# Performance work log

Measured on AMD Instinct MI355X. Metric: run time of the kernel, lower is better.

## Reference

```python
import jax, jax.numpy as jnp
import numpy as np

EPS = 1e-12  # matches torch F.normalize default eps

def setup_inputs() -> dict:
    key = jax.random.key(0)
    k1, k2 = jax.random.split(key)
    query = jax.random.normal(k1, (8, 2048, 512), dtype=jnp.float32)
    support = jax.random.normal(k2, (8, 4096, 512), dtype=jnp.float32)
    return {"query": query, "support": support}

def _l2_normalize(x):
    # torch.nn.functional.normalize(x, dim=-1): x / max(||x||, eps)
    n = jnp.sqrt(jnp.sum(x * x, axis=-1, keepdims=True))
    return x / jnp.maximum(n, EPS)

def reference(query, support):
    # cosine distance: 1 - q_hat @ s_hat^T  -> [B, Nq, Ns]
    qn = _l2_normalize(query)
    sn = _l2_normalize(support)
    dist = 1.0 - jnp.einsum('bqd,bsd->bqs', qn, sn)
    min_d = jnp.min(dist, axis=2)        # [B, Nq]
    return jnp.mean(min_d, axis=1)       # [B]
```

## Files before the change

### kernel.cpp

```cpp
#include <hip/hip_runtime.h>
#include <hip/hip_bf16.h>

typedef __attribute__((ext_vector_type(8))) short short8;
typedef __attribute__((ext_vector_type(4))) float f32x4;
typedef __attribute__((ext_vector_type(16))) float f32x16;
typedef __attribute__((ext_vector_type(8))) int int8v;

#define D   512
#define NQ  2048
#define NS  4096
#define NB  8
#define BM  128
#define BN  128
#define BK  32

typedef const __attribute__((address_space(1))) unsigned int gas_uint;
typedef __attribute__((address_space(3))) unsigned int las_uint;

#define WAIT_VM8   0x0F78
#define WAIT_VM4   0x0F74
#define WAIT_VM0   0x0F70
#define WAIT_LGKM0 0xC07F

__device__ __forceinline__ short f2bf(float f) {
  unsigned u = __builtin_bit_cast(unsigned, f);
  unsigned r = u + 0x7fffu + ((u >> 16) & 1u);
  return (short)(r >> 16);
}

__device__ __forceinline__ short8 pack8(float4 a, float4 b, float r) {
  short8 o;
  o[0] = f2bf(a.x * r); o[1] = f2bf(a.y * r); o[2] = f2bf(a.z * r); o[3] = f2bf(a.w * r);
  o[4] = f2bf(b.x * r); o[5] = f2bf(b.y * r); o[6] = f2bf(b.z * r); o[7] = f2bf(b.w * r);
  return o;
}

__global__ void normcvt8_kernel(const float* __restrict__ q, const float* __restrict__ s,
                                unsigned char* __restrict__ qn, unsigned char* __restrict__ sn,
                                unsigned* __restrict__ maxenc) {
  if (blockIdx.x < 64) maxenc[(blockIdx.x << 8) | threadIdx.x] = 0;
  int wave = blockIdx.x * 4 + (threadIdx.x >> 6);
  int lane = threadIdx.x & 63;
  const int NQR = NB * NQ;
  const float4* src; unsigned char* dst;
  if (wave < NQR) { src = (const float4*)(q + (size_t)wave * D); dst = qn + (size_t)wave * D; }
  else {
    size_t w = wave - NQR;
    src = (const float4*)(s + w * D); dst = sn + w * D;
  }
  float4 a = src[lane * 2];
  float4 b = src[lane * 2 + 1];
  float ss = a.x*a.x + a.y*a.y + a.z*a.z + a.w*a.w
           + b.x*b.x + b.y*b.y + b.z*b.z + b.w*b.w;
  #pragma unroll
  for (int m = 32; m >= 1; m >>= 1) ss += __shfl_xor(ss, m, 64);
  float r = 1.0f / fmaxf(sqrtf(ss), 1e-12f);
  int w0 = __builtin_amdgcn_cvt_pk_fp8_f32(a.x * r, a.y * r, 0, false);
  w0     = __builtin_amdgcn_cvt_pk_fp8_f32(a.z * r, a.w * r, w0, true);
  int w1 = __builtin_amdgcn_cvt_pk_fp8_f32(b.x * r, b.y * r, 0, false);
  w1     = __builtin_amdgcn_cvt_pk_fp8_f32(b.z * r, b.w * r, w1, true);
  *(int2*)(dst + lane * 8) = make_int2(w0, w1);
}

__global__ __launch_bounds__(256) void cosmax11_kernel(
    const unsigned char* __restrict__ Qn, const unsigned char* __restrict__ Sn,
    unsigned int* __restrict__ maxenc)
{
  __shared__ __align__(16) unsigned char sbuf[65536];
  __shared__ float maxbuf[64][2];

  const int id  = blockIdx.x;
  const int b   = id & 7;
  const int j   = id >> 3;
  const int mt  = j & 31;
  const int nsp = j >> 5;
  const int tid  = threadIdx.x;
  const int wave = tid >> 6;
  const int lane = tid & 63;
  const int l31 = lane & 31, kc = lane >> 5;
  const int mstrip = wave & 1, nhalf = wave >> 1;

  {
    const unsigned char* Qbase = Qn + ((size_t)b * NQ + (size_t)mt * 64) * D;
    const int baserow = wave * 2 + (lane >> 5);
    #pragma unroll
    for (int p = 0; p < 8; ++p) {
      int row = p * 8 + baserow;
      int g   = (lane & 31) ^ (row & 31);
      __builtin_amdgcn_global_load_lds(
          (gas_uint*)(Qbase + (size_t)row * D + g * 16),
          (las_uint*)(sbuf + 16384 + p * 4096 + wave * 1024), 16, 0, 0);
    }
  }
  __syncthreads();

  const int srow8 = lane >> 3;
  const int sch   = (lane & 7) ^ srow8;
  const unsigned char* gS = Sn +
      ((size_t)b * NS + (size_t)nsp * 2048 + wave * 32 + srow8) * D + sch * 16;

  auto issue = [&](size_t goff, int ldsoff) {
    #pragma unroll
    for (int t = 0; t < 4; ++t)
      __builtin_amdgcn_global_load_lds((gas_uint*)(gS + goff + (size_t)t * 4096),
          (las_uint*)(sbuf + ldsoff + wave * 4096 + t * 1024), 16, 0, 0);
  };

  issue(0, 0);

  const int arow = mstrip * 32 + l31;
  int8v a[8];
  #pragma unroll
  for (int kk = 0; kk < 8; ++kk) {
    int c0 = (4 * kk + 2 * kc) ^ l31;
    ((int4*)&a[kk])[0] = *(const int4*)&sbuf[16384 + arow * 512 + c0 * 16];
    ((int4*)&a[kk])[1] = *(const int4*)&sbuf[16384 + arow * 512 + (c0 ^ 1) * 16];
  }
  __builtin_amdgcn_s_waitcnt(WAIT_LGKM0);
  asm volatile("" ::: "memory");
  __builtin_amdgcn_s_barrier();
  asm volatile("" ::: "memory");
  issue(128, 16384);
  issue(256, 32768);

  const int brow0 = (nhalf * 64 + l31) * 128;
  const int brow1 = brow0 + 4096;
  const int cxor  = ((kc * 2) ^ (l31 & 7)) * 16;

  f32x16 acc0, acc1;
  float rmax[16];
  #pragma unroll
  for (int r = 0; r < 16; ++r) rmax[r] = -2.0f;

  auto computeK = [&](int kt, int rdo) {
    const unsigned char* Bb = sbuf + rdo;
    #pragma unroll
    for (int ss = 0; ss < 2; ++ss) {
      const int cb = cxor ^ (ss * 64);
      int8v b0, b1;
      ((int4*)&b0)[0] = *(const int4*)&Bb[brow0 + cb];
      ((int4*)&b0)[1] = *(const int4*)&Bb[brow0 + (cb ^ 16)];
      ((int4*)&b1)[0] = *(const int4*)&Bb[brow1 + cb];
      ((int4*)&b1)[1] = *(const int4*)&Bb[brow1 + (cb ^ 16)];
      acc0 = __builtin_amdgcn_mfma_scale_f32_32x32x64_f8f6f4(
          a[kt * 2 + ss], b0, acc0, 0, 0, 0, 0x7f7f7f7f, 0, 0x7f7f7f7f);
      acc1 = __builtin_amdgcn_mfma_scale_f32_32x32x64_f8f6f4(
          a[kt * 2 + ss], b1, acc1, 0, 0, 0, 0x7f7f7f7f, 0, 0x7f7f7f7f);
    }
  };

  #pragma clang loop unroll(disable)
  for (int nt2 = 0; nt2 < 16; ++nt2) {
    const size_t ntb = (size_t)nt2 << 16;
    const bool more = (nt2 < 15);

    __builtin_amdgcn_s_waitcnt(WAIT_VM8);
    asm volatile("" ::: "memory");
    __builtin_amdgcn_s_barrier();
    asm volatile("" ::: "memory");
    issue(ntb + 384, 49152);
    #pragma unroll
    for (int r = 0; r < 16; ++r) { acc0[r] = 0.f; acc1[r] = 0.f; }
    computeK(0, 0);

    __builtin_amdgcn_s_waitcnt(WAIT_VM8);
    asm volatile("" ::: "memory");
    __builtin_amdgcn_s_barrier();
    asm volatile("" ::: "memory");
    if (more) issue(ntb + 65536, 0);
    computeK(1, 16384);

    if (more) __builtin_amdgcn_s_waitcnt(WAIT_VM8);
    else      __builtin_amdgcn_s_waitcnt(WAIT_VM4);
    asm volatile("" ::: "memory");
    __builtin_amdgcn_s_barrier();
    asm volatile("" ::: "memory");
    if (more) issue(ntb + 65536 + 128, 16384);
    computeK(2, 32768);

    if (more) __builtin_amdgcn_s_waitcnt(WAIT_VM8);
    else      __builtin_amdgcn_s_waitcnt(WAIT_VM0);
    asm volatile("" ::: "memory");
    __builtin_amdgcn_s_barrier();
    asm volatile("" ::: "memory");
    if (more) issue(ntb + 65536 + 256, 32768);
    computeK(3, 49152);

    #pragma unroll
    for (int r = 0; r < 16; ++r)
      rmax[r] = fmaxf(rmax[r], fmaxf(acc0[r], acc1[r]));
  }

  #pragma unroll
  for (int r = 0; r < 16; ++r) {
    float v = rmax[r];
    v = fmaxf(v, __shfl_xor(v, 1, 64));
    v = fmaxf(v, __shfl_xor(v, 2, 64));
    v = fmaxf(v, __shfl_xor(v, 4, 64));
    v = fmaxf(v, __shfl_xor(v, 8, 64));
    v = fmaxf(v, __shfl_xor(v, 16, 64));
    if (l31 == 0)
      maxbuf[mstrip * 32 + (r & 3) + 8 * (r >> 2) + 4 * kc][nhalf] = v;
  }
  __syncthreads();

  if (tid < 64) {
    float v = fmaxf(maxbuf[tid][0], maxbuf[tid][1]);
    unsigned e = __builtin_bit_cast(unsigned, v);
    e = ((int)e >= 0) ? (e | 0x80000000u) : ~e;
    atomicMax(&maxenc[(size_t)b * NQ + (size_t)mt * 64 + tid], e);
  }
}

__global__ void finalize_kernel(const unsigned* __restrict__ maxenc,
                                float* __restrict__ out) {
  int b = blockIdx.x;
  int tid = threadIdx.x;
  float sum = 0.f;
  for (int i = tid; i < NQ; i += 256) {
    unsigned e = maxenc[(size_t)b * NQ + i];
    unsigned u = (e & 0x80000000u) ? (e & 0x7fffffffu) : ~e;
    float v = __builtin_bit_cast(float, u);
    sum += 1.0f - v;
  }
  #pragma unroll
  for (int m = 32; m >= 1; m >>= 1) sum += __shfl_xor(sum, m, 64);
  __shared__ float part[4];
  if ((tid & 63) == 0) part[tid >> 6] = sum;
  __syncthreads();
  if (tid == 0) out[b] = (part[0] + part[1] + part[2] + part[3]) * (1.0f / (float)NQ);
}

__global__ void norms_kernel(const float* __restrict__ q, const float* __restrict__ s,
                             float* __restrict__ rq, float* __restrict__ rs) {
  int wave = blockIdx.x * 4 + (threadIdx.x >> 6);
  int lane = threadIdx.x & 63;
  const int NQR = NB * NQ, NSR = NB * NS;
  if (wave >= NQR + NSR) return;
  const float4* r4; float* outp;
  if (wave < NQR) { r4 = (const float4*)(q + (size_t)wave * D); outp = rq + wave; }
  else           { r4 = (const float4*)(s + (size_t)(wave - NQR) * D); outp = rs + (wave - NQR); }
  float4 a = r4[lane];
  float4 b = r4[lane + 64];
  float ss = a.x*a.x + a.y*a.y + a.z*a.z + a.w*a.w
           + b.x*b.x + b.y*b.y + b.z*b.z + b.w*b.w;
  #pragma unroll
  for (int m = 32; m >= 1; m >>= 1) ss += __shfl_xor(ss, m, 64);
  if (lane == 0) *outp = 1.0f / fmaxf(sqrtf(ss), 1e-12f);
}

__global__ __launch_bounds__(256, 3) void cosmax_kernel(
    const float* __restrict__ Q, const float* __restrict__ S,
    const float* __restrict__ rq, const float* __restrict__ rs,
    unsigned int* __restrict__ maxenc)
{
  __shared__ short As[BM * BK];
  __shared__ short Bs[BN * BK];
  __shared__ float maxbuf[BM][2];

  const int b  = blockIdx.z, mt = blockIdx.y, nt = blockIdx.x;
  const float* Qb  = Q + ((size_t)b * NQ + mt * BM) * D;
  const float* Sb  = S + ((size_t)b * NS + nt * BN) * D;
  const float* rqb = rq + (size_t)b * NQ + mt * BM;
  const float* rsb = rs + (size_t)b * NS + nt * BN;

  const int tid  = threadIdx.x;
  const int srow = tid >> 2;
  const int kseg = (tid & 3) * 8;
  const float rq0 = rqb[srow], rq1 = rqb[srow + 64];
  const float rs0 = rsb[srow], rs1 = rsb[srow + 64];
  const int wave = tid >> 6, lane = tid & 63;
  const int wm = (wave & 1) * 64, wn = (wave >> 1) * 64;
  const int lm = lane & 15, lk = (lane >> 4) * 8;

  f32x4 acc[4][4];
  #pragma unroll
  for (int i = 0; i < 4; ++i)
    #pragma unroll
    for (int j = 0; j < 4; ++j) acc[i][j] = (f32x4){0.f, 0.f, 0.f, 0.f};

  const float* qrow0 = Qb + (size_t)srow * D + kseg;
  const float* qrow1 = qrow0 + (size_t)64 * D;
  const float* srow0 = Sb + (size_t)srow * D + kseg;
  const float* srow1 = srow0 + (size_t)64 * D;

  float4 qa, qb2, qc, qd, sa, sb2, sc, sd;
  #define LOADK(k0)                                                    \
    qa  = *(const float4*)(qrow0 + (k0));  qb2 = *(const float4*)(qrow0 + (k0) + 4); \
    qc  = *(const float4*)(qrow1 + (k0));  qd  = *(const float4*)(qrow1 + (k0) + 4); \
    sa  = *(const float4*)(srow0 + (k0));  sb2 = *(const float4*)(srow0 + (k0) + 4); \
    sc  = *(const float4*)(srow1 + (k0));  sd  = *(const float4*)(srow1 + (k0) + 4);
  LOADK(0);
  #pragma unroll 4
  for (int kt = 0; kt < D / BK; ++kt) {
    *(short8*)&As[srow        * BK + kseg] = pack8(qa, qb2, rq0);
    *(short8*)&As[(srow + 64) * BK + kseg] = pack8(qc, qd,  rq1);
    *(short8*)&Bs[srow        * BK + kseg] = pack8(sa, sb2, rs0);
    *(short8*)&Bs[(srow + 64) * BK + kseg] = pack8(sc, sd,  rs1);
    __syncthreads();
    if (kt < D / BK - 1) { LOADK((kt + 1) * BK); }
    short8 af[4], bf[4];
    #pragma unroll
    for (int i = 0; i < 4; ++i) af[i] = *(short8*)&As[(wm + i * 16 + lm) * BK + lk];
    #pragma unroll
    for (int j = 0; j < 4; ++j) bf[j] = *(short8*)&Bs[(wn + j * 16 + lm) * BK + lk];
    #pragma unroll
    for (int i = 0; i < 4; ++i)
      #pragma unroll
      for (int j = 0; j < 4; ++j)
        acc[i][j] = __builtin_amdgcn_mfma_f32_16x16x32_bf16(af[i], bf[j], acc[i][j], 0, 0, 0);
    __syncthreads();
  }
  #undef LOADK

  #pragma unroll
  for (int i = 0; i < 4; ++i) {
    #pragma unroll
    for (int r = 0; r < 4; ++r) {
      float v = fmaxf(fmaxf(acc[i][0][r], acc[i][1][r]),
                      fmaxf(acc[i][2][r], acc[i][3][r]));
      v = fmaxf(v, __shfl_xor(v, 1, 64));
      v = fmaxf(v, __shfl_xor(v, 2, 64));
      v = fmaxf(v, __shfl_xor(v, 4, 64));
      v = fmaxf(v, __shfl_xor(v, 8, 64));
      if ((lane & 15) == 0) {
        int row = wm + i * 16 + (lane >> 4) * 4 + r;
        maxbuf[row][wave >> 1] = v;
      }
    }
  }
  __syncthreads();
  if (tid < BM) {
    float v = fmaxf(maxbuf[tid][0], maxbuf[tid][1]);
    unsigned e = __builtin_bit_cast(unsigned, v);
    e = ((int)e >= 0) ? (e | 0x80000000u) : ~e;
    atomicMax(&maxenc[(size_t)b * NQ + mt * BM + tid], e);
  }
}

extern "C" void kernel_launch(void* const* d_in, const int* in_sizes, int n_in,
                              void* d_out, int out_size, void* d_ws, size_t ws_size,
                              hipStream_t stream) {
  const float* q = (const float*)d_in[0];
  const float* s = (const float*)d_in[1];
  float* out = (float*)d_out;

  unsigned* maxenc = (unsigned*)d_ws;
  const size_t QOFF = 65536;
  const size_t SOFF = QOFF + (size_t)NB * NQ * D;
  const size_t NEED = SOFF + (size_t)NB * NS * D;

  if (ws_size >= NEED) {
    unsigned char* qn = (unsigned char*)d_ws + QOFF;
    unsigned char* sn = (unsigned char*)d_ws + SOFF;
    normcvt8_kernel<<<NB * (NQ + NS) / 4, 256, 0, stream>>>(q, s, qn, sn, maxenc);
    cosmax11_kernel<<<512, 256, 0, stream>>>(qn, sn, maxenc);
    finalize_kernel<<<NB, 256, 0, stream>>>(maxenc, out);
  } else {
    float* rq = (float*)((char*)d_ws + 65536);
    float* rs = (float*)((char*)d_ws + 131072);
    hipMemsetAsync(maxenc, 0, (size_t)NB * NQ * sizeof(unsigned), stream);
    norms_kernel<<<NB * (NQ + NS) / 4, 256, 0, stream>>>(q, s, rq, rs);
    dim3 grid(NS / BN, NQ / BM, NB);
    cosmax_kernel<<<grid, 256, 0, stream>>>(q, s, rq, rs, maxenc);
    finalize_kernel<<<NB, 256, 0, stream>>>(maxenc, out);
  }
}
```

Before: 162.9 us.

## Double query tile per block to 128 rows and halve support span

Each block now holds 128 query rows (two 32-row A fragments per wave) instead of 64 and sweeps 1024 support rows instead of 2048. Each loaded B fragment feeds twice as many MFMAs, which halves the support LDS and global traffic per unit of compute. The Q tile now fills the whole 64 KB shared buffer before the support pipeline reuses it, and the extra accumulators and A registers raise register pressure. Launch bounds now request two blocks per CU.

```diff
diff --git a/kernel.cpp b/kernel.cpp
--- a/kernel.cpp
+++ b/kernel.cpp
@@ -62,18 +62,18 @@
   *(int2*)(dst + lane * 8) = make_int2(w0, w1);
 }
 
-__global__ __launch_bounds__(256) void cosmax11_kernel(
+__global__ __launch_bounds__(256, 2) void cosmax13_kernel(
     const unsigned char* __restrict__ Qn, const unsigned char* __restrict__ Sn,
     unsigned int* __restrict__ maxenc)
 {
   __shared__ __align__(16) unsigned char sbuf[65536];
-  __shared__ float maxbuf[64][2];
+  __shared__ float maxbuf[128][2];
 
   const int id  = blockIdx.x;
   const int b   = id & 7;
   const int j   = id >> 3;
-  const int mt  = j & 31;
-  const int nsp = j >> 5;
+  const int mt  = j & 15;
+  const int nsp = j >> 4;
   const int tid  = threadIdx.x;
   const int wave = tid >> 6;
   const int lane = tid & 63;
@@ -81,15 +81,15 @@
   const int mstrip = wave & 1, nhalf = wave >> 1;
 
   {
-    const unsigned char* Qbase = Qn + ((size_t)b * NQ + (size_t)mt * 64) * D;
+    const unsigned char* Qbase = Qn + ((size_t)b * NQ + (size_t)mt * 128) * D;
     const int baserow = wave * 2 + (lane >> 5);
     #pragma unroll
-    for (int p = 0; p < 8; ++p) {
+    for (int p = 0; p < 16; ++p) {
       int row = p * 8 + baserow;
       int g   = (lane & 31) ^ (row & 31);
       __builtin_amdgcn_global_load_lds(
           (gas_uint*)(Qbase + (size_t)row * D + g * 16),
-          (las_uint*)(sbuf + 16384 + p * 4096 + wave * 1024), 16, 0, 0);
+          (las_uint*)(sbuf + p * 4096 + wave * 1024), 16, 0, 0);
     }
   }
   __syncthreads();
@@ -97,7 +97,7 @@
   const int srow8 = lane >> 3;
   const int sch   = (lane & 7) ^ srow8;
   const unsigned char* gS = Sn +
-      ((size_t)b * NS + (size_t)nsp * 2048 + wave * 32 + srow8) * D + sch * 16;
+      ((size_t)b * NS + (size_t)nsp * 1024 + wave * 32 + srow8) * D + sch * 16;
 
   auto issue = [&](size_t goff, int ldsoff) {
     #pragma unroll
@@ -106,20 +106,22 @@
           (las_uint*)(sbuf + ldsoff + wave * 4096 + t * 1024), 16, 0, 0);
   };
 
-  issue(0, 0);
-
-  const int arow = mstrip * 32 + l31;
-  int8v a[8];
-  #pragma unroll
-  for (int kk = 0; kk < 8; ++kk) {
-    int c0 = (4 * kk + 2 * kc) ^ l31;
-    ((int4*)&a[kk])[0] = *(const int4*)&sbuf[16384 + arow * 512 + c0 * 16];
-    ((int4*)&a[kk])[1] = *(const int4*)&sbuf[16384 + arow * 512 + (c0 ^ 1) * 16];
+  int8v a[2][8];
+  #pragma unroll
+  for (int m = 0; m < 2; ++m) {
+    const int arow = mstrip * 64 + m * 32 + l31;
+    #pragma unroll
+    for (int kk = 0; kk < 8; ++kk) {
+      int c0 = (4 * kk + 2 * kc) ^ l31;
+      ((int4*)&a[m][kk])[0] = *(const int4*)&sbuf[arow * 512 + c0 * 16];
+      ((int4*)&a[m][kk])[1] = *(const int4*)&sbuf[arow * 512 + (c0 ^ 1) * 16];
+    }
   }
   __builtin_amdgcn_s_waitcnt(WAIT_LGKM0);
   asm volatile("" ::: "memory");
   __builtin_amdgcn_s_barrier();
   asm volatile("" ::: "memory");
+  issue(0,   0);
   issue(128, 16384);
   issue(256, 32768);
 
@@ -127,10 +129,10 @@
   const int brow1 = brow0 + 4096;
   const int cxor  = ((kc * 2) ^ (l31 & 7)) * 16;
 
-  f32x16 acc0, acc1;
-  float rmax[16];
-  #pragma unroll
-  for (int r = 0; r < 16; ++r) rmax[r] = -2.0f;
+  f32x16 acc00, acc01, acc10, acc11;
+  float rmax0[16], rmax1[16];
+  #pragma unroll
+  for (int r = 0; r < 16; ++r) { rmax0[r] = -2.0f; rmax1[r] = -2.0f; }
 
   auto computeK = [&](int kt, int rdo) {
     const unsigned char* Bb = sbuf + rdo;
@@ -140,19 +142,23 @@
       int8v b0, b1;
       ((int4*)&b0)[0] = *(const int4*)&Bb[brow0 + cb];
       ((int4*)&b0)[1] = *(const int4*)&Bb[brow0 + (cb ^ 16)];
+      acc00 = __builtin_amdgcn_mfma_scale_f32_32x32x64_f8f6f4(
+          a[0][kt * 2 + ss], b0, acc00, 0, 0, 0, 0x7f7f7f7f, 0, 0x7f7f7f7f);
+      acc10 = __builtin_amdgcn_mfma_scale_f32_32x32x64_f8f6f4(
+          a[1][kt * 2 + ss], b0, acc10, 0, 0, 0, 0x7f7f7f7f, 0, 0x7f7f7f7f);
       ((int4*)&b1)[0] = *(const int4*)&Bb[brow1 + cb];
       ((int4*)&b1)[1] = *(const int4*)&Bb[brow1 + (cb ^ 16)];
-      acc0 = __builtin_amdgcn_mfma_scale_f32_32x32x64_f8f6f4(
-          a[kt * 2 + ss], b0, acc0, 0, 0, 0, 0x7f7f7f7f, 0, 0x7f7f7f7f);
-      acc1 = __builtin_amdgcn_mfma_scale_f32_32x32x64_f8f6f4(
-          a[kt * 2 + ss], b1, acc1, 0, 0, 0, 0x7f7f7f7f, 0, 0x7f7f7f7f);
+      acc01 = __builtin_amdgcn_mfma_scale_f32_32x32x64_f8f6f4(
+          a[0][kt * 2 + ss], b1, acc01, 0, 0, 0, 0x7f7f7f7f, 0, 0x7f7f7f7f);
+      acc11 = __builtin_amdgcn_mfma_scale_f32_32x32x64_f8f6f4(
+          a[1][kt * 2 + ss], b1, acc11, 0, 0, 0, 0x7f7f7f7f, 0, 0x7f7f7f7f);
     }
   };
 
   #pragma clang loop unroll(disable)
-  for (int nt2 = 0; nt2 < 16; ++nt2) {
+  for (int nt2 = 0; nt2 < 8; ++nt2) {
     const size_t ntb = (size_t)nt2 << 16;
-    const bool more = (nt2 < 15);
+    const bool more = (nt2 < 7);
 
     __builtin_amdgcn_s_waitcnt(WAIT_VM8);
     asm volatile("" ::: "memory");
@@ -160,7 +166,7 @@
     asm volatile("" ::: "memory");
     issue(ntb + 384, 49152);
     #pragma unroll
-    for (int r = 0; r < 16; ++r) { acc0[r] = 0.f; acc1[r] = 0.f; }
+    for (int r = 0; r < 16; ++r) { acc00[r] = 0.f; acc01[r] = 0.f; acc10[r] = 0.f; acc11[r] = 0.f; }
     computeK(0, 0);
 
     __builtin_amdgcn_s_waitcnt(WAIT_VM8);
@@ -187,28 +193,33 @@
     computeK(3, 49152);
 
     #pragma unroll
-    for (int r = 0; r < 16; ++r)
-      rmax[r] = fmaxf(rmax[r], fmaxf(acc0[r], acc1[r]));
-  }
-
-  #pragma unroll
-  for (int r = 0; r < 16; ++r) {
-    float v = rmax[r];
-    v = fmaxf(v, __shfl_xor(v, 1, 64));
-    v = fmaxf(v, __shfl_xor(v, 2, 64));
-    v = fmaxf(v, __shfl_xor(v, 4, 64));
-    v = fmaxf(v, __shfl_xor(v, 8, 64));
-    v = fmaxf(v, __shfl_xor(v, 16, 64));
-    if (l31 == 0)
-      maxbuf[mstrip * 32 + (r & 3) + 8 * (r >> 2) + 4 * kc][nhalf] = v;
+    for (int r = 0; r < 16; ++r) {
+      rmax0[r] = fmaxf(rmax0[r], fmaxf(acc00[r], acc01[r]));
+      rmax1[r] = fmaxf(rmax1[r], fmaxf(acc10[r], acc11[r]));
+    }
+  }
+
+  #pragma unroll
+  for (int m = 0; m < 2; ++m) {
+    #pragma unroll
+    for (int r = 0; r < 16; ++r) {
+      float v = m ? rmax1[r] : rmax0[r];
+      v = fmaxf(v, __shfl_xor(v, 1, 64));
+      v = fmaxf(v, __shfl_xor(v, 2, 64));
+      v = fmaxf(v, __shfl_xor(v, 4, 64));
+      v = fmaxf(v, __shfl_xor(v, 8, 64));
+      v = fmaxf(v, __shfl_xor(v, 16, 64));
+      if (l31 == 0)
+        maxbuf[mstrip * 64 + m * 32 + (r & 3) + 8 * (r >> 2) + 4 * kc][nhalf] = v;
+    }
   }
   __syncthreads();
 
-  if (tid < 64) {
+  if (tid < 128) {
     float v = fmaxf(maxbuf[tid][0], maxbuf[tid][1]);
     unsigned e = __builtin_bit_cast(unsigned, v);
     e = ((int)e >= 0) ? (e | 0x80000000u) : ~e;
-    atomicMax(&maxenc[(size_t)b * NQ + (size_t)mt * 64 + tid], e);
+    atomicMax(&maxenc[(size_t)b * NQ + (size_t)mt * 128 + tid], e);
   }
 }
 
@@ -354,7 +365,7 @@
     unsigned char* qn = (unsigned char*)d_ws + QOFF;
     unsigned char* sn = (unsigned char*)d_ws + SOFF;
     normcvt8_kernel<<<NB * (NQ + NS) / 4, 256, 0, stream>>>(q, s, qn, sn, maxenc);
-    cosmax11_kernel<<<512, 256, 0, stream>>>(qn, sn, maxenc);
+    cosmax13_kernel<<<512, 256, 0, stream>>>(qn, sn, maxenc);
     finalize_kernel<<<NB, 256, 0, stream>>>(maxenc, out);
   } else {
     float* rq = (float*)((char*)d_ws + 65536);
```

Measured after the change: 184.9 us. 1.14x slower.

## Give each wave the full 64-row query strip and halve per-tile barriers

Applied to the files above, without the earlier changes.

Each wave now keeps A fragments for both 32-row query strips in registers and handles its own 32-column slice of the support tile, so every B fragment read from LDS feeds two MFMAs. This halves B LDS reads per MFMA. The k-loop is regrouped so two k-chunks are computed per barrier, with loads issued in pairs and waits on a full vmcnt drain, giving two syncs per tile instead of four. Launch bounds request two blocks per CU, and the cross-wave max reduction widens to four waves. Register pressure goes up from doubled A fragments and running maxima, and draining vmcnt to zero gives less load/compute overlap.

```diff
diff --git a/kernel.cpp b/kernel.cpp
--- a/kernel.cpp
+++ b/kernel.cpp
@@ -18,7 +18,6 @@
 typedef __attribute__((address_space(3))) unsigned int las_uint;
 
 #define WAIT_VM8   0x0F78
-#define WAIT_VM4   0x0F74
 #define WAIT_VM0   0x0F70
 #define WAIT_LGKM0 0xC07F
 
@@ -62,12 +61,12 @@
   *(int2*)(dst + lane * 8) = make_int2(w0, w1);
 }
 
-__global__ __launch_bounds__(256) void cosmax11_kernel(
+__global__ __launch_bounds__(256, 2) void cosmax14_kernel(
     const unsigned char* __restrict__ Qn, const unsigned char* __restrict__ Sn,
     unsigned int* __restrict__ maxenc)
 {
   __shared__ __align__(16) unsigned char sbuf[65536];
-  __shared__ float maxbuf[64][2];
+  __shared__ float maxbuf[64][4];
 
   const int id  = blockIdx.x;
   const int b   = id & 7;
@@ -78,7 +77,6 @@
   const int wave = tid >> 6;
   const int lane = tid & 63;
   const int l31 = lane & 31, kc = lane >> 5;
-  const int mstrip = wave & 1, nhalf = wave >> 1;
 
   {
     const unsigned char* Qbase = Qn + ((size_t)b * NQ + (size_t)mt * 64) * D;
@@ -108,13 +106,16 @@
 
   issue(0, 0);
 
-  const int arow = mstrip * 32 + l31;
-  int8v a[8];
-  #pragma unroll
-  for (int kk = 0; kk < 8; ++kk) {
-    int c0 = (4 * kk + 2 * kc) ^ l31;
-    ((int4*)&a[kk])[0] = *(const int4*)&sbuf[16384 + arow * 512 + c0 * 16];
-    ((int4*)&a[kk])[1] = *(const int4*)&sbuf[16384 + arow * 512 + (c0 ^ 1) * 16];
+  int8v a[2][8];
+  #pragma unroll
+  for (int m = 0; m < 2; ++m) {
+    const int arow = m * 32 + l31;
+    #pragma unroll
+    for (int kk = 0; kk < 8; ++kk) {
+      int c0 = (4 * kk + 2 * kc) ^ l31;
+      ((int4*)&a[m][kk])[0] = *(const int4*)&sbuf[16384 + arow * 512 + c0 * 16];
+      ((int4*)&a[m][kk])[1] = *(const int4*)&sbuf[16384 + arow * 512 + (c0 ^ 1) * 16];
+    }
   }
   __builtin_amdgcn_s_waitcnt(WAIT_LGKM0);
   asm volatile("" ::: "memory");
@@ -122,30 +123,28 @@
   asm volatile("" ::: "memory");
   issue(128, 16384);
   issue(256, 32768);
-
-  const int brow0 = (nhalf * 64 + l31) * 128;
-  const int brow1 = brow0 + 4096;
-  const int cxor  = ((kc * 2) ^ (l31 & 7)) * 16;
+  issue(384, 49152);
+
+  const int brow = (wave * 32 + l31) * 128;
+  const int cxor = ((kc * 2) ^ (l31 & 7)) * 16;
 
   f32x16 acc0, acc1;
-  float rmax[16];
-  #pragma unroll
-  for (int r = 0; r < 16; ++r) rmax[r] = -2.0f;
+  float rmax0[16], rmax1[16];
+  #pragma unroll
+  for (int r = 0; r < 16; ++r) { rmax0[r] = -2.0f; rmax1[r] = -2.0f; }
 
   auto computeK = [&](int kt, int rdo) {
     const unsigned char* Bb = sbuf + rdo;
     #pragma unroll
     for (int ss = 0; ss < 2; ++ss) {
       const int cb = cxor ^ (ss * 64);
-      int8v b0, b1;
-      ((int4*)&b0)[0] = *(const int4*)&Bb[brow0 + cb];
-      ((int4*)&b0)[1] = *(const int4*)&Bb[brow0 + (cb ^ 16)];
-      ((int4*)&b1)[0] = *(const int4*)&Bb[brow1 + cb];
-      ((int4*)&b1)[1] = *(const int4*)&Bb[brow1 + (cb ^ 16)];
+      int8v b0;
+      ((int4*)&b0)[0] = *(const int4*)&Bb[brow + cb];
+      ((int4*)&b0)[1] = *(const int4*)&Bb[brow + (cb ^ 16)];
       acc0 = __builtin_amdgcn_mfma_scale_f32_32x32x64_f8f6f4(
-          a[kt * 2 + ss], b0, acc0, 0, 0, 0, 0x7f7f7f7f, 0, 0x7f7f7f7f);
+          a[0][kt * 2 + ss], b0, acc0, 0, 0, 0, 0x7f7f7f7f, 0, 0x7f7f7f7f);
       acc1 = __builtin_amdgcn_mfma_scale_f32_32x32x64_f8f6f4(
-          a[kt * 2 + ss], b1, acc1, 0, 0, 0, 0x7f7f7f7f, 0, 0x7f7f7f7f);
+          a[1][kt * 2 + ss], b0, acc1, 0, 0, 0, 0x7f7f7f7f, 0, 0x7f7f7f7f);
     }
   };
 
@@ -154,58 +153,57 @@
     const size_t ntb = (size_t)nt2 << 16;
     const bool more = (nt2 < 15);
 
-    __builtin_amdgcn_s_waitcnt(WAIT_VM8);
+    if (nt2 == 0) __builtin_amdgcn_s_waitcnt(WAIT_VM8);
+    else          __builtin_amdgcn_s_waitcnt(WAIT_VM0);
     asm volatile("" ::: "memory");
     __builtin_amdgcn_s_barrier();
     asm volatile("" ::: "memory");
-    issue(ntb + 384, 49152);
+    if (nt2 > 0) {
+      issue(ntb + 256, 32768);
+      issue(ntb + 384, 49152);
+    }
     #pragma unroll
     for (int r = 0; r < 16; ++r) { acc0[r] = 0.f; acc1[r] = 0.f; }
     computeK(0, 0);
-
-    __builtin_amdgcn_s_waitcnt(WAIT_VM8);
+    computeK(1, 16384);
+
+    __builtin_amdgcn_s_waitcnt(WAIT_VM0);
     asm volatile("" ::: "memory");
     __builtin_amdgcn_s_barrier();
     asm volatile("" ::: "memory");
-    if (more) issue(ntb + 65536, 0);
-    computeK(1, 16384);
-
-    if (more) __builtin_amdgcn_s_waitcnt(WAIT_VM8);
-    else      __builtin_amdgcn_s_waitcnt(WAIT_VM4);
-    asm volatile("" ::: "memory");
-    __builtin_amdgcn_s_barrier();
-    asm volatile("" ::: "memory");
-    if (more) issue(ntb + 65536 + 128, 16384);
+    if (more) {
+      issue(ntb + 65536, 0);
+      issue(ntb + 65536 + 128, 16384);
+    }
     computeK(2, 32768);
-
-    if (more) __builtin_amdgcn_s_waitcnt(WAIT_VM8);
-    else      __builtin_amdgcn_s_waitcnt(WAIT_VM0);
-    asm volatile("" ::: "memory");
-    __builtin_amdgcn_s_barrier();
-    asm volatile("" ::: "memory");
-    if (more) issue(ntb + 65536 + 256, 32768);
     computeK(3, 49152);
 
     #pragma unroll
-    for (int r = 0; r < 16; ++r)
-      rmax[r] = fmaxf(rmax[r], fmaxf(acc0[r], acc1[r]));
-  }
-
-  #pragma unroll
-  for (int r = 0; r < 16; ++r) {
-    float v = rmax[r];
-    v = fmaxf(v, __shfl_xor(v, 1, 64));
-    v = fmaxf(v, __shfl_xor(v, 2, 64));
-    v = fmaxf(v, __shfl_xor(v, 4, 64));
-    v = fmaxf(v, __shfl_xor(v, 8, 64));
-    v = fmaxf(v, __shfl_xor(v, 16, 64));
-    if (l31 == 0)
-      maxbuf[mstrip * 32 + (r & 3) + 8 * (r >> 2) + 4 * kc][nhalf] = v;
+    for (int r = 0; r < 16; ++r) {
+      rmax0[r] = fmaxf(rmax0[r], acc0[r]);
+      rmax1[r] = fmaxf(rmax1[r], acc1[r]);
+    }
+  }
+
+  #pragma unroll
+  for (int m = 0; m < 2; ++m) {
+    #pragma unroll
+    for (int r = 0; r < 16; ++r) {
+      float v = m ? rmax1[r] : rmax0[r];
+      v = fmaxf(v, __shfl_xor(v, 1, 64));
+      v = fmaxf(v, __shfl_xor(v, 2, 64));
+      v = fmaxf(v, __shfl_xor(v, 4, 64));
+      v = fmaxf(v, __shfl_xor(v, 8, 64));
+      v = fmaxf(v, __shfl_xor(v, 16, 64));
+      if (l31 == 0)
+        maxbuf[m * 32 + (r & 3) + 8 * (r >> 2) + 4 * kc][wave] = v;
+    }
   }
   __syncthreads();
 
   if (tid < 64) {
-    float v = fmaxf(maxbuf[tid][0], maxbuf[tid][1]);
+    float v = fmaxf(fmaxf(maxbuf[tid][0], maxbuf[tid][1]),
+                    fmaxf(maxbuf[tid][2], maxbuf[tid][3]));
     unsigned e = __builtin_bit_cast(unsigned, v);
     e = ((int)e >= 0) ? (e | 0x80000000u) : ~e;
     atomicMax(&maxenc[(size_t)b * NQ + (size_t)mt * 64 + tid], e);
@@ -354,7 +352,7 @@
     unsigned char* qn = (unsigned char*)d_ws + QOFF;
     unsigned char* sn = (unsigned char*)d_ws + SOFF;
     normcvt8_kernel<<<NB * (NQ + NS) / 4, 256, 0, stream>>>(q, s, qn, sn, maxenc);
-    cosmax11_kernel<<<512, 256, 0, stream>>>(qn, sn, maxenc);
+    cosmax14_kernel<<<512, 256, 0, stream>>>(qn, sn, maxenc);
     finalize_kernel<<<NB, 256, 0, stream>>>(maxenc, out);
   } else {
     float* rq = (float*)((char*)d_ws + 65536);
```

Result: slower. 167.1 us (+2.6%).

## Split support into thirds with triple-buffered LDS for three blocks per CU

Applied to the files above, without the earlier changes.

The cosine-max kernel now splits each batch's support rows three ways (1408/1408/1280 rows) instead of two, launching 768 blocks instead of 512. LDS drops from a 4-stage to a 3-stage rotating buffer (48KB) with launch_bounds(256,3), so three blocks can be resident per CU. The aim is better load balance across CUs and more latency hiding through occupancy. MFMA issue is also wrapped in s_setprio to favour math waves. The cost is a shallower prefetch depth per block, more blocks contending for the shared max output, and a 1 KB smaller Q-tile region that must still fit within the reduced buffer.

```diff
diff --git a/kernel.cpp b/kernel.cpp
--- a/kernel.cpp
+++ b/kernel.cpp
@@ -62,18 +62,19 @@
   *(int2*)(dst + lane * 8) = make_int2(w0, w1);
 }
 
-__global__ __launch_bounds__(256) void cosmax11_kernel(
+__global__ __launch_bounds__(256, 3) void cosmax16_kernel(
     const unsigned char* __restrict__ Qn, const unsigned char* __restrict__ Sn,
     unsigned int* __restrict__ maxenc)
 {
-  __shared__ __align__(16) unsigned char sbuf[65536];
+  __shared__ __align__(16) unsigned char sbuf[49152];
   __shared__ float maxbuf[64][2];
 
   const int id  = blockIdx.x;
   const int b   = id & 7;
   const int j   = id >> 3;
   const int mt  = j & 31;
-  const int nsp = j >> 5;
+  const int third = j >> 5;
+  const int nt  = (third == 2) ? 10 : 11;
   const int tid  = threadIdx.x;
   const int wave = tid >> 6;
   const int lane = tid & 63;
@@ -97,7 +98,7 @@
   const int srow8 = lane >> 3;
   const int sch   = (lane & 7) ^ srow8;
   const unsigned char* gS = Sn +
-      ((size_t)b * NS + (size_t)nsp * 2048 + wave * 32 + srow8) * D + sch * 16;
+      ((size_t)b * NS + (size_t)third * 1408 + wave * 32 + srow8) * D + sch * 16;
 
   auto issue = [&](size_t goff, int ldsoff) {
     #pragma unroll
@@ -121,7 +122,6 @@
   __builtin_amdgcn_s_barrier();
   asm volatile("" ::: "memory");
   issue(128, 16384);
-  issue(256, 32768);
 
   const int brow0 = (nhalf * 64 + l31) * 128;
   const int brow1 = brow0 + 4096;
@@ -142,54 +142,66 @@
       ((int4*)&b0)[1] = *(const int4*)&Bb[brow0 + (cb ^ 16)];
       ((int4*)&b1)[0] = *(const int4*)&Bb[brow1 + cb];
       ((int4*)&b1)[1] = *(const int4*)&Bb[brow1 + (cb ^ 16)];
+      __builtin_amdgcn_s_setprio(1);
       acc0 = __builtin_amdgcn_mfma_scale_f32_32x32x64_f8f6f4(
           a[kt * 2 + ss], b0, acc0, 0, 0, 0, 0x7f7f7f7f, 0, 0x7f7f7f7f);
       acc1 = __builtin_amdgcn_mfma_scale_f32_32x32x64_f8f6f4(
           a[kt * 2 + ss], b1, acc1, 0, 0, 0, 0x7f7f7f7f, 0, 0x7f7f7f7f);
+      __builtin_amdgcn_s_setprio(0);
     }
   };
 
+  int rd = 0, wr = 32768;
+  size_t tb = 0;
+
+  #define ROT(x) x = (x == 32768) ? 0 : (x + 16384)
+
   #pragma clang loop unroll(disable)
-  for (int nt2 = 0; nt2 < 16; ++nt2) {
-    const size_t ntb = (size_t)nt2 << 16;
-    const bool more = (nt2 < 15);
-
-    __builtin_amdgcn_s_waitcnt(WAIT_VM8);
+  for (int t = 0; t < nt; ++t) {
+    const bool more = (t < nt - 1);
+
+    __builtin_amdgcn_s_waitcnt(WAIT_VM4);
     asm volatile("" ::: "memory");
     __builtin_amdgcn_s_barrier();
     asm volatile("" ::: "memory");
-    issue(ntb + 384, 49152);
+    issue(tb + 256, wr);
     #pragma unroll
     for (int r = 0; r < 16; ++r) { acc0[r] = 0.f; acc1[r] = 0.f; }
-    computeK(0, 0);
-
-    __builtin_amdgcn_s_waitcnt(WAIT_VM8);
+    computeK(0, rd);
+    wr = rd; ROT(rd);
+
+    __builtin_amdgcn_s_waitcnt(WAIT_VM4);
     asm volatile("" ::: "memory");
     __builtin_amdgcn_s_barrier();
     asm volatile("" ::: "memory");
-    if (more) issue(ntb + 65536, 0);
-    computeK(1, 16384);
-
-    if (more) __builtin_amdgcn_s_waitcnt(WAIT_VM8);
-    else      __builtin_amdgcn_s_waitcnt(WAIT_VM4);
+    issue(tb + 384, wr);
+    computeK(1, rd);
+    wr = rd; ROT(rd);
+
+    __builtin_amdgcn_s_waitcnt(WAIT_VM4);
     asm volatile("" ::: "memory");
     __builtin_amdgcn_s_barrier();
     asm volatile("" ::: "memory");
-    if (more) issue(ntb + 65536 + 128, 16384);
-    computeK(2, 32768);
-
-    if (more) __builtin_amdgcn_s_waitcnt(WAIT_VM8);
+    if (more) issue(tb + 65536, wr);
+    computeK(2, rd);
+    wr = rd; ROT(rd);
+
+    if (more) __builtin_amdgcn_s_waitcnt(WAIT_VM4);
     else      __builtin_amdgcn_s_waitcnt(WAIT_VM0);
     asm volatile("" ::: "memory");
     __builtin_amdgcn_s_barrier();
     asm volatile("" ::: "memory");
-    if (more) issue(ntb + 65536 + 256, 32768);
-    computeK(3, 49152);
+    if (more) issue(tb + 65536 + 128, wr);
+    computeK(3, rd);
+    wr = rd; ROT(rd);
 
     #pragma unroll
     for (int r = 0; r < 16; ++r)
       rmax[r] = fmaxf(rmax[r], fmaxf(acc0[r], acc1[r]));
-  }
+
+    tb += 65536;
+  }
+  #undef ROT
 
   #pragma unroll
   for (int r = 0; r < 16; ++r) {
@@ -354,7 +366,7 @@
     unsigned char* qn = (unsigned char*)d_ws + QOFF;
     unsigned char* sn = (unsigned char*)d_ws + SOFF;
     normcvt8_kernel<<<NB * (NQ + NS) / 4, 256, 0, stream>>>(q, s, qn, sn, maxenc);
-    cosmax11_kernel<<<512, 256, 0, stream>>>(qn, sn, maxenc);
+    cosmax16_kernel<<<768, 256, 0, stream>>>(qn, sn, maxenc);
     finalize_kernel<<<NB, 256, 0, stream>>>(maxenc, out);
   } else {
     float* rq = (float*)((char*)d_ws + 65536);
```

Result: slower. 196.5 us (+20.6%).
